# Optimization experiments

Measured on AMD Instinct MI355X. Metric: run time of the kernel, lower is better.

## Reference

```python
import jax, jax.numpy as jnp
import numpy as np

N = 100000
NEG_SLOPE = 0.2


def gat_conv(x, edge_index, W, att_src, att_dst, bias, heads, out_ch, concat):
    # x: [N, F_in]; W: [F_in, heads*out_ch]; att_*: [heads, out_ch]; bias per PyG
    h = (x @ W).reshape(N, heads, out_ch)  # [N, H, C]
    # add self loops (PyG default add_self_loops=True)
    loop = jnp.arange(N, dtype=edge_index.dtype)
    src = jnp.concatenate([edge_index[0], loop])  # [E+N]
    dst = jnp.concatenate([edge_index[1], loop])
    a_src = jnp.einsum('nhc,hc->nh', h, att_src)  # [N, H]
    a_dst = jnp.einsum('nhc,hc->nh', h, att_dst)
    e = jax.nn.leaky_relu(a_src[src] + a_dst[dst], NEG_SLOPE)  # [E+N, H]
    # segment softmax over destination nodes (numerically stable)
    m = jax.ops.segment_max(e, dst, num_segments=N)
    e = jnp.exp(e - m[dst])
    denom = jax.ops.segment_sum(e, dst, num_segments=N)
    alpha = e / (denom[dst] + 1e-16)  # [E+N, H]
    # weighted scatter-add aggregation
    out = jax.ops.segment_sum(h[src] * alpha[:, :, None], dst, num_segments=N)  # [N,H,C]
    if concat:
        out = out.reshape(N, heads * out_ch)
    else:
        out = out.mean(axis=1)
    return out + bias


def setup_inputs() -> dict:
    key = jax.random.key(0)
    ks = jax.random.split(key, 10)
    F_in, H1, C1, NCLS = 512, 8, 8, 40
    E = 1600000
    x = jax.random.normal(ks[0], (N, F_in), dtype=jnp.float32)
    edge_index = jax.random.randint(ks[1], (2, E), 0, N, dtype=jnp.int64)
    s1 = 1.0 / np.sqrt(F_in)
    s2 = 1.0 / np.sqrt(H1 * C1)
    return {
        'x': x,
        'edge_index': edge_index,
        'W1': jax.random.normal(ks[2], (F_in, H1 * C1), dtype=jnp.float32) * s1,
        'att_src1': jax.random.normal(ks[3], (H1, C1), dtype=jnp.float32) * 0.1,
        'att_dst1': jax.random.normal(ks[4], (H1, C1), dtype=jnp.float32) * 0.1,
        'b1': jnp.zeros((H1 * C1,), dtype=jnp.float32),
        'W2': jax.random.normal(ks[5], (H1 * C1, NCLS), dtype=jnp.float32) * s2,
        'att_src2': jax.random.normal(ks[6], (1, NCLS), dtype=jnp.float32) * 0.1,
        'att_dst2': jax.random.normal(ks[7], (1, NCLS), dtype=jnp.float32) * 0.1,
        'b2': jnp.zeros((NCLS,), dtype=jnp.float32),
    }


def reference(x, edge_index, W1, att_src1, att_dst1, b1, W2, att_src2, att_dst2, b2):
    # dropout in eval mode -> identity
    h = gat_conv(x, edge_index, W1, att_src1, att_dst1, b1, heads=8, out_ch=8, concat=True)
    h = jax.nn.elu(h)
    NCLS = W2.shape[1]
    out = gat_conv(h, edge_index, W2, att_src2, att_dst2, b2, heads=1, out_ch=NCLS, concat=False)
    return jax.nn.softmax(out, axis=1)
```

## Files before the change

### kernel.cpp

```cpp
#include <hip/hip_runtime.h>
#include <math.h>

#define N_NODES 100000
#define FIN     512
#define H1H     8
#define C1C     8
#define HC1     64
#define NCLS    40
#define NEG_SLOPE 0.2f

#define NPB   256
#define NBUK  391
#define EPB   4096

#define TM 64
#define BK 16
#define XPAD 68

__global__ __launch_bounds__(256) void k_gemm1(const float* __restrict__ x,
                                               const float* __restrict__ W1,
                                               const float* __restrict__ att_src,
                                               const float* __restrict__ att_dst,
                                               float* __restrict__ h1,
                                               float* __restrict__ a_src,
                                               float* __restrict__ a_dst) {
    __shared__ float xs[2][BK][XPAD];
    const int tx   = threadIdx.x;
    const int lane = tx & 63;
    const int wid  = __builtin_amdgcn_readfirstlane(tx >> 6);
    const int c0   = wid << 4;
    const int row_base = blockIdx.x * TM;
    const int gr   = row_base + lane;
    const bool valid = gr < N_NODES;

    const int sr  = tx >> 2;
    const int sk  = (tx & 3) << 2;
    const int sgr = row_base + sr;
    const bool svalid = sgr < N_NODES;

    float4 xr4;
    auto load_regs = [&](int k0) {
        xr4 = svalid ? *(const float4*)(x + (size_t)sgr * FIN + k0 + sk)
                     : make_float4(0.f, 0.f, 0.f, 0.f);
    };
    auto store_lds = [&](int buf) {
        xs[buf][sk + 0][sr] = xr4.x;
        xs[buf][sk + 1][sr] = xr4.y;
        xs[buf][sk + 2][sr] = xr4.z;
        xs[buf][sk + 3][sr] = xr4.w;
    };

    float acc[16];
#pragma unroll
    for (int j = 0; j < 16; j++) acc[j] = 0.f;

    load_regs(0);
    store_lds(0);
    __syncthreads();

    int buf = 0;
    for (int k0 = 0; k0 < FIN; k0 += BK, buf ^= 1) {
        const bool more = (k0 + BK < FIN);
        if (more) load_regs(k0 + BK);
#pragma unroll
        for (int k = 0; k < BK; k++) {
            const float xv = xs[buf][k][lane];
            const float* wr = W1 + (size_t)(k0 + k) * HC1 + c0;
#pragma unroll
            for (int j = 0; j < 16; j++)
                acc[j] = fmaf(xv, wr[j], acc[j]);
        }
        if (more) {
            store_lds(buf ^ 1);
            __syncthreads();
        }
    }

    float s0 = 0.f, s1 = 0.f, d0 = 0.f, d1 = 0.f;
#pragma unroll
    for (int j = 0; j < 8; j++) {
        s0 = fmaf(acc[j],     att_src[c0 + j],     s0);
        d0 = fmaf(acc[j],     att_dst[c0 + j],     d0);
        s1 = fmaf(acc[8 + j], att_src[c0 + 8 + j], s1);
        d1 = fmaf(acc[8 + j], att_dst[c0 + 8 + j], d1);
    }
    if (valid) {
#pragma unroll
        for (int t = 0; t < 4; t++)
            *(float4*)(h1 + (size_t)gr * HC1 + c0 + 4 * t) =
                make_float4(acc[4 * t], acc[4 * t + 1], acc[4 * t + 2], acc[4 * t + 3]);
        const int h0 = wid * 2;
        a_src[gr * H1H + h0]     = s0;
        a_src[gr * H1H + h0 + 1] = s1;
        a_dst[gr * H1H + h0]     = d0;
        a_dst[gr * H1H + h0 + 1] = d1;
    }
}

__global__ __launch_bounds__(256) void k_bcnt(const int* __restrict__ dst, int E,
                                              int* __restrict__ gcnt) {
    __shared__ int lcnt[NBUK];
    for (int i = threadIdx.x; i < NBUK; i += 256) lcnt[i] = 0;
    __syncthreads();
    const int e0 = blockIdx.x * EPB;
#pragma unroll
    for (int i = 0; i < EPB / 256; i++) {
        const int e = e0 + i * 256 + threadIdx.x;
        if (e < E) atomicAdd(&lcnt[dst[e] >> 8], 1);
    }
    __syncthreads();
    for (int i = threadIdx.x; i < NBUK; i += 256)
        if (lcnt[i]) atomicAdd(&gcnt[i], lcnt[i]);
}

__global__ __launch_bounds__(512) void k_bscan(const int* __restrict__ gcnt,
                                               int* __restrict__ gbase,
                                               int* __restrict__ gcur, int E) {
    __shared__ int sm[512];
    const int t = threadIdx.x;
    const int v = (t < NBUK) ? gcnt[t] : 0;
    sm[t] = v;
    __syncthreads();
    for (int off = 1; off < 512; off <<= 1) {
        const int u = (t >= off) ? sm[t - off] : 0;
        __syncthreads();
        sm[t] += u;
        __syncthreads();
    }
    if (t < NBUK) {
        const int b = sm[t] - v;
        gbase[t] = b;
        gcur[t]  = b;
    }
    if (t == 0) gbase[NBUK] = E;
}

__global__ __launch_bounds__(256) void k_bfill(const int* __restrict__ src,
                                               const int* __restrict__ dst, int E,
                                               int* __restrict__ gcur,
                                               int2* __restrict__ pairs) {
    __shared__ int lcnt[NBUK];
    __shared__ int lbase[NBUK];
    for (int i = threadIdx.x; i < NBUK; i += 256) lcnt[i] = 0;
    __syncthreads();
    const int e0 = blockIdx.x * EPB;
#pragma unroll
    for (int i = 0; i < EPB / 256; i++) {
        const int e = e0 + i * 256 + threadIdx.x;
        if (e < E) atomicAdd(&lcnt[dst[e] >> 8], 1);
    }
    __syncthreads();
    for (int i = threadIdx.x; i < NBUK; i += 256)
        lbase[i] = lcnt[i] ? atomicAdd(&gcur[i], lcnt[i]) : 0;
    __syncthreads();
#pragma unroll
    for (int i = 0; i < EPB / 256; i++) {
        const int e = e0 + i * 256 + threadIdx.x;
        if (e < E) {
            const int d = dst[e];
            const int pos = atomicAdd(&lbase[d >> 8], 1);
            pairs[pos] = make_int2(src[e], d);
        }
    }
}

__global__ __launch_bounds__(256) void k_bscatter(const int2* __restrict__ pairs,
                                                  const int* __restrict__ gbase,
                                                  int* __restrict__ offs,
                                                  int* __restrict__ srcsort, int E) {
    __shared__ int ldeg[NPB];
    __shared__ int ltmp[NPB];
    __shared__ int lcur[NPB];
    const int b = blockIdx.x;
    const int tx = threadIdx.x;
    const int node0 = b << 8;
    const int pbeg = gbase[b];
    const int cnt  = gbase[b + 1] - pbeg;

    ldeg[tx] = 0;
    __syncthreads();
    for (int i = tx; i < cnt; i += 256)
        atomicAdd(&ldeg[pairs[pbeg + i].y - node0], 1);
    __syncthreads();
    const int v = ldeg[tx];
    ltmp[tx] = v;
    __syncthreads();
    for (int off = 1; off < 256; off <<= 1) {
        const int u = (tx >= off) ? ltmp[tx - off] : 0;
        __syncthreads();
        ltmp[tx] += u;
        __syncthreads();
    }
    const int mypos = pbeg + ltmp[tx] - v;
    if (node0 + tx < N_NODES) offs[node0 + tx] = mypos;
    lcur[tx] = mypos;
    if (b == NBUK - 1 && tx == 0) offs[N_NODES] = E;
    __syncthreads();
    for (int i = tx; i < cnt; i += 256) {
        const int2 p = pairs[pbeg + i];
        const int pos = atomicAdd(&lcur[p.y - node0], 1);
        srcsort[pos] = p.x;
    }
}

__global__ __launch_bounds__(256) void k_agg1(const float* __restrict__ h1,
                                              const float* __restrict__ a_src,
                                              const float* __restrict__ a_dst,
                                              const int* __restrict__ offs,
                                              const int* __restrict__ srcsort,
                                              const float* __restrict__ b1,
                                              float* __restrict__ h1e) {
    const int n = blockIdx.x * 4 + (threadIdx.x >> 6);
    if (n >= N_NODES) return;
    const int lane = threadIdx.x & 63;
    const int hh   = lane >> 3;
    const float adn = a_dst[n * H1H + hh];
    const int beg = offs[n], end = offs[n + 1];

    float e0 = a_src[n * H1H + hh] + adn;
    e0 = e0 > 0.f ? e0 : NEG_SLOPE * e0;
    float m = e0;
    float denom = 1.f;
    float acc = h1[(size_t)n * HC1 + lane];

    int j = beg;
    for (; j + 8 <= end; j += 8) {
        int s[8];
#pragma unroll
        for (int t = 0; t < 8; t++) s[t] = srcsort[j + t];
        float q[8], g[8];
#pragma unroll
        for (int t = 0; t < 8; t++) q[t] = a_src[s[t] * H1H + hh];
#pragma unroll
        for (int t = 0; t < 8; t++) g[t] = h1[(size_t)s[t] * HC1 + lane];
        float f[8];
#pragma unroll
        for (int t = 0; t < 8; t++) {
            const float e = q[t] + adn;
            f[t] = e > 0.f ? e : NEG_SLOPE * e;
        }
        const float cm = fmaxf(fmaxf(fmaxf(f[0], f[1]), fmaxf(f[2], f[3])),
                               fmaxf(fmaxf(f[4], f[5]), fmaxf(f[6], f[7])));
        const float nm = fmaxf(m, cm);
        const float sc = __expf(m - nm);
        float w[8];
#pragma unroll
        for (int t = 0; t < 8; t++) w[t] = __expf(f[t] - nm);
        const float wsum = ((w[0] + w[1]) + (w[2] + w[3])) + ((w[4] + w[5]) + (w[6] + w[7]));
        const float wg = fmaf(w[0], g[0], fmaf(w[1], g[1], fmaf(w[2], g[2], fmaf(w[3], g[3],
                         fmaf(w[4], g[4], fmaf(w[5], g[5], fmaf(w[6], g[6], w[7] * g[7])))))));
        denom = fmaf(denom, sc, wsum);
        acc = fmaf(acc, sc, wg);
        m = nm;
    }
    for (; j + 4 <= end; j += 4) {
        const int s0 = srcsort[j], s1 = srcsort[j + 1];
        const int s2 = srcsort[j + 2], s3 = srcsort[j + 3];
        const float q0 = a_src[s0 * H1H + hh], q1 = a_src[s1 * H1H + hh];
        const float q2 = a_src[s2 * H1H + hh], q3 = a_src[s3 * H1H + hh];
        const float g0 = h1[(size_t)s0 * HC1 + lane];
        const float g1 = h1[(size_t)s1 * HC1 + lane];
        const float g2 = h1[(size_t)s2 * HC1 + lane];
        const float g3 = h1[(size_t)s3 * HC1 + lane];
        float f0 = q0 + adn; f0 = f0 > 0.f ? f0 : NEG_SLOPE * f0;
        float f1 = q1 + adn; f1 = f1 > 0.f ? f1 : NEG_SLOPE * f1;
        float f2 = q2 + adn; f2 = f2 > 0.f ? f2 : NEG_SLOPE * f2;
        float f3 = q3 + adn; f3 = f3 > 0.f ? f3 : NEG_SLOPE * f3;
        const float nm = fmaxf(m, fmaxf(fmaxf(f0, f1), fmaxf(f2, f3)));
        const float sc = __expf(m - nm);
        const float w0 = __expf(f0 - nm), w1 = __expf(f1 - nm);
        const float w2 = __expf(f2 - nm), w3 = __expf(f3 - nm);
        denom = fmaf(denom, sc, (w0 + w1) + (w2 + w3));
        acc = fmaf(acc, sc, fmaf(w0, g0, fmaf(w1, g1, fmaf(w2, g2, w3 * g3))));
        m = nm;
    }
    for (; j < end; j++) {
        const int s = srcsort[j];
        float e = a_src[s * H1H + hh] + adn;
        e = e > 0.f ? e : NEG_SLOPE * e;
        const float g = h1[(size_t)s * HC1 + lane];
        const float nm = fmaxf(m, e);
        const float sc = __expf(m - nm);
        const float w = __expf(e - nm);
        denom = fmaf(denom, sc, w);
        acc = fmaf(acc, sc, w * g);
        m = nm;
    }
    float v = acc / denom + b1[lane];
    h1e[(size_t)n * HC1 + lane] = v > 0.f ? v : (__expf(v) - 1.f);
}

#define TM2 128
__global__ __launch_bounds__(256) void k_gemm2(const float* __restrict__ h1e,
                                               const float* __restrict__ W2,
                                               const float* __restrict__ att_src2,
                                               const float* __restrict__ att_dst2,
                                               float* __restrict__ h2,
                                               float* __restrict__ a_src2,
                                               float* __restrict__ a_dst2) {
    __shared__ float hs[32][65][4];
    __shared__ float w2t[NCLS][68];
    __shared__ float asv[NCLS], adv[NCLS];
    const int tx = threadIdx.x;
    const int node0 = blockIdx.x * TM2;

    for (int f = tx; f < HC1 * NCLS; f += 256) {
        const int k = f / NCLS, c = f - k * NCLS;
        w2t[c][k] = W2[f];
    }
    if (tx < NCLS) {
        asv[tx] = att_src2[tx];
        adv[tx] = att_dst2[tx];
    }
#pragma unroll
    for (int i = 0; i < 8; i++) {
        const int f  = tx + 256 * i;
        const int n  = f >> 4;
        const int k4 = (f & 15) << 2;
        const int gn = node0 + n;
        const float4 v = (gn < N_NODES) ? *(const float4*)(h1e + (size_t)gn * HC1 + k4)
                                        : make_float4(0.f, 0.f, 0.f, 0.f);
        const int ng = n >> 2, ni = n & 3;
        hs[ng][k4 + 0][ni] = v.x;
        hs[ng][k4 + 1][ni] = v.y;
        hs[ng][k4 + 2][ni] = v.z;
        hs[ng][k4 + 3][ni] = v.w;
    }
    __syncthreads();

    const int ng = tx >> 3;
    const int cg = tx & 7;
    const int c0 = cg * 5;

    float acc[4][5];
#pragma unroll
    for (int i = 0; i < 4; i++)
#pragma unroll
        for (int j = 0; j < 5; j++) acc[i][j] = 0.f;

    for (int k = 0; k < HC1; k += 4) {
        float4 hv[4];
#pragma unroll
        for (int t = 0; t < 4; t++) hv[t] = *(const float4*)&hs[ng][k + t][0];
#pragma unroll
        for (int j = 0; j < 5; j++) {
            const float4 wv = *(const float4*)&w2t[c0 + j][k];
            acc[0][j] = fmaf(hv[0].x, wv.x, fmaf(hv[1].x, wv.y, fmaf(hv[2].x, wv.z, fmaf(hv[3].x, wv.w, acc[0][j]))));
            acc[1][j] = fmaf(hv[0].y, wv.x, fmaf(hv[1].y, wv.y, fmaf(hv[2].y, wv.z, fmaf(hv[3].y, wv.w, acc[1][j]))));
            acc[2][j] = fmaf(hv[0].z, wv.x, fmaf(hv[1].z, wv.y, fmaf(hv[2].z, wv.z, fmaf(hv[3].z, wv.w, acc[2][j]))));
            acc[3][j] = fmaf(hv[0].w, wv.x, fmaf(hv[1].w, wv.y, fmaf(hv[2].w, wv.z, fmaf(hv[3].w, wv.w, acc[3][j]))));
        }
    }

    float ps[4], pd[4];
#pragma unroll
    for (int i = 0; i < 4; i++) {
        const int gn = node0 + ng * 4 + i;
        float s = 0.f, d = 0.f;
#pragma unroll
        for (int j = 0; j < 5; j++) {
            s = fmaf(acc[i][j], asv[c0 + j], s);
            d = fmaf(acc[i][j], adv[c0 + j], d);
        }
        ps[i] = s;
        pd[i] = d;
        if (gn < N_NODES) {
#pragma unroll
            for (int j = 0; j < 5; j++)
                h2[(size_t)gn * NCLS + c0 + j] = acc[i][j];
        }
    }
#pragma unroll
    for (int off = 1; off < 8; off <<= 1) {
#pragma unroll
        for (int i = 0; i < 4; i++) {
            ps[i] += __shfl_xor(ps[i], off, 64);
            pd[i] += __shfl_xor(pd[i], off, 64);
        }
    }
    if (cg == 0) {
#pragma unroll
        for (int i = 0; i < 4; i++) {
            const int gn = node0 + ng * 4 + i;
            if (gn < N_NODES) {
                a_src2[gn] = ps[i];
                a_dst2[gn] = pd[i];
            }
        }
    }
}

__global__ __launch_bounds__(256) void k_agg2(const float* __restrict__ h2,
                                              const float* __restrict__ a_src,
                                              const float* __restrict__ a_dst,
                                              const int* __restrict__ offs,
                                              const int* __restrict__ srcsort,
                                              const float* __restrict__ b2,
                                              float* __restrict__ out) {
    const int n = blockIdx.x * 4 + (threadIdx.x >> 6);
    if (n >= N_NODES) return;
    const int lane = threadIdx.x & 63;
    const float adn = a_dst[n];
    const int beg = offs[n], end = offs[n + 1];

    float e0 = a_src[n] + adn;
    e0 = e0 > 0.f ? e0 : NEG_SLOPE * e0;
    float m = e0;
    float denom = 1.f;
    float acc = (lane < NCLS) ? h2[(size_t)n * NCLS + lane] : 0.f;

    int j = beg;
    for (; j + 8 <= end; j += 8) {
        int s[8];
#pragma unroll
        for (int t = 0; t < 8; t++) s[t] = srcsort[j + t];
        float q[8], g[8];
#pragma unroll
        for (int t = 0; t < 8; t++) q[t] = a_src[s[t]];
#pragma unroll
        for (int t = 0; t < 8; t++)
            g[t] = (lane < NCLS) ? h2[(size_t)s[t] * NCLS + lane] : 0.f;
        float f[8];
#pragma unroll
        for (int t = 0; t < 8; t++) {
            const float e = q[t] + adn;
            f[t] = e > 0.f ? e : NEG_SLOPE * e;
        }
        const float cm = fmaxf(fmaxf(fmaxf(f[0], f[1]), fmaxf(f[2], f[3])),
                               fmaxf(fmaxf(f[4], f[5]), fmaxf(f[6], f[7])));
        const float nm = fmaxf(m, cm);
        const float sc = __expf(m - nm);
        float w[8];
#pragma unroll
        for (int t = 0; t < 8; t++) w[t] = __expf(f[t] - nm);
        const float wsum = ((w[0] + w[1]) + (w[2] + w[3])) + ((w[4] + w[5]) + (w[6] + w[7]));
        const float wg = fmaf(w[0], g[0], fmaf(w[1], g[1], fmaf(w[2], g[2], fmaf(w[3], g[3],
                         fmaf(w[4], g[4], fmaf(w[5], g[5], fmaf(w[6], g[6], w[7] * g[7])))))));
        denom = fmaf(denom, sc, wsum);
        acc = fmaf(acc, sc, wg);
        m = nm;
    }
    for (; j + 4 <= end; j += 4) {
        const int s0 = srcsort[j], s1 = srcsort[j + 1];
        const int s2 = srcsort[j + 2], s3 = srcsort[j + 3];
        const float q0 = a_src[s0], q1 = a_src[s1];
        const float q2 = a_src[s2], q3 = a_src[s3];
        float g0 = 0.f, g1 = 0.f, g2 = 0.f, g3 = 0.f;
        if (lane < NCLS) {
            g0 = h2[(size_t)s0 * NCLS + lane];
            g1 = h2[(size_t)s1 * NCLS + lane];
            g2 = h2[(size_t)s2 * NCLS + lane];
            g3 = h2[(size_t)s3 * NCLS + lane];
        }
        float f0 = q0 + adn; f0 = f0 > 0.f ? f0 : NEG_SLOPE * f0;
        float f1 = q1 + adn; f1 = f1 > 0.f ? f1 : NEG_SLOPE * f1;
        float f2 = q2 + adn; f2 = f2 > 0.f ? f2 : NEG_SLOPE * f2;
        float f3 = q3 + adn; f3 = f3 > 0.f ? f3 : NEG_SLOPE * f3;
        const float nm = fmaxf(m, fmaxf(fmaxf(f0, f1), fmaxf(f2, f3)));
        const float sc = __expf(m - nm);
        const float w0 = __expf(f0 - nm), w1 = __expf(f1 - nm);
        const float w2 = __expf(f2 - nm), w3 = __expf(f3 - nm);
        denom = fmaf(denom, sc, (w0 + w1) + (w2 + w3));
        acc = fmaf(acc, sc, fmaf(w0, g0, fmaf(w1, g1, fmaf(w2, g2, w3 * g3))));
        m = nm;
    }
    for (; j < end; j++) {
        const int s = srcsort[j];
        float e = a_src[s] + adn;
        e = e > 0.f ? e : NEG_SLOPE * e;
        const float g = (lane < NCLS) ? h2[(size_t)s * NCLS + lane] : 0.f;
        const float nm = fmaxf(m, e);
        const float sc = __expf(m - nm);
        const float w = __expf(e - nm);
        denom = fmaf(denom, sc, w);
        acc = fmaf(acc, sc, w * g);
        m = nm;
    }
    float o = (lane < NCLS) ? (acc / denom + b2[lane]) : -INFINITY;
    float mx = o;
#pragma unroll
    for (int off = 32; off; off >>= 1) mx = fmaxf(mx, __shfl_xor(mx, off, 64));
    const float ex = (lane < NCLS) ? __expf(o - mx) : 0.f;
    float sm = ex;
#pragma unroll
    for (int off = 32; off; off >>= 1) sm += __shfl_xor(sm, off, 64);
    if (lane < NCLS) out[(size_t)n * NCLS + lane] = ex / sm;
}

extern "C" void kernel_launch(void* const* d_in, const int* in_sizes, int n_in,
                              void* d_out, int out_size, void* d_ws, size_t ws_size,
                              hipStream_t stream) {
    const float* x   = (const float*)d_in[0];
    const int*   ei  = (const int*)d_in[1];
    const float* W1v = (const float*)d_in[2];
    const float* as1 = (const float*)d_in[3];
    const float* ad1 = (const float*)d_in[4];
    const float* b1  = (const float*)d_in[5];
    const float* W2v = (const float*)d_in[6];
    const float* as2 = (const float*)d_in[7];
    const float* ad2 = (const float*)d_in[8];
    const float* b2  = (const float*)d_in[9];
    const int E = in_sizes[1] / 2;
    const int* esrc = ei;
    const int* edst = ei + E;

    char* wp = (char*)d_ws;
    auto alloc = [&](size_t bytes) {
        char* p = wp;
        wp += (bytes + 255) & ~(size_t)255;
        return p;
    };
    float* h1     = (float*)alloc((size_t)N_NODES * HC1 * 4);
    float* h1e    = (float*)alloc((size_t)N_NODES * HC1 * 4);
    float* a_src1 = (float*)alloc((size_t)N_NODES * H1H * 4);
    float* a_dst1 = (float*)alloc((size_t)N_NODES * H1H * 4);
    float* a_src2 = (float*)alloc((size_t)N_NODES * 4);
    float* a_dst2 = (float*)alloc((size_t)N_NODES * 4);
    int*   offs   = (int*)alloc((size_t)(N_NODES + 1) * 4);
    int*   gcnt   = (int*)alloc((size_t)NBUK * 4);
    int*   gbase  = (int*)alloc((size_t)(NBUK + 1) * 4);
    int*   gcur   = (int*)alloc((size_t)NBUK * 4);
    int*   srcsort= (int*)alloc((size_t)E * 4);
    int2*  pairs  = (int2*)alloc((size_t)E * 8);
    float* h2     = h1;

    hipMemsetAsync(gcnt, 0, (size_t)NBUK * 4, stream);

    const int NEB = (E + EPB - 1) / EPB;
    k_gemm1<<<(N_NODES + TM - 1) / TM, 256, 0, stream>>>(x, W1v, as1, ad1, h1, a_src1, a_dst1);
    k_bcnt<<<NEB, 256, 0, stream>>>(edst, E, gcnt);
    k_bscan<<<1, 512, 0, stream>>>(gcnt, gbase, gcur, E);
    k_bfill<<<NEB, 256, 0, stream>>>(esrc, edst, E, gcur, pairs);
    k_bscatter<<<NBUK, 256, 0, stream>>>(pairs, gbase, offs, srcsort, E);
    k_agg1<<<(N_NODES + 3) / 4, 256, 0, stream>>>(h1, a_src1, a_dst1, offs, srcsort, b1, h1e);
    k_gemm2<<<(N_NODES + TM2 - 1) / TM2, 256, 0, stream>>>(h1e, W2v, as2, ad2, h2, a_src2, a_dst2);
    k_agg2<<<(N_NODES + 3) / 4, 256, 0, stream>>>(h2, a_src2, a_dst2, offs, srcsort, b2, (float*)d_out);
}
```

Baseline: 661.2 us.

## Register-tile first-layer GEMM with 16x8 outputs per thread and LDS-staged weights

Rewrites the first projection GEMM so each thread computes a 16-row by 8-column register tile. The block tile grows to 256 rows with 128 threads, and both x and W1 are staged in double-buffered LDS with padded, swizzled rows. Before, every thread read 16 W1 values from global memory per k step and did only 16 FMAs per LDS load; the new tiling raises FMA-to-load intensity. The cost is heavy register pressure (128 accumulators), fewer blocks (391) and lower occupancy.

Measured after the change: 654.9 us. Within noise of the previous version (-0.9%).

```diff
diff --git a/kernel.cpp b/kernel.cpp
--- a/kernel.cpp
+++ b/kernel.cpp
@@ -13,46 +13,63 @@
 #define NBUK  391
 #define EPB   4096
 
-#define TM 64
-#define BK 16
-#define XPAD 68
-
-__global__ __launch_bounds__(256) void k_gemm1(const float* __restrict__ x,
+#define TM 256
+#define BK 8
+#define XSW 320
+
+__global__ __launch_bounds__(128) void k_gemm1(const float* __restrict__ x,
                                                const float* __restrict__ W1,
                                                const float* __restrict__ att_src,
                                                const float* __restrict__ att_dst,
                                                float* __restrict__ h1,
                                                float* __restrict__ a_src,
                                                float* __restrict__ a_dst) {
-    __shared__ float xs[2][BK][XPAD];
-    const int tx   = threadIdx.x;
-    const int lane = tx & 63;
-    const int wid  = __builtin_amdgcn_readfirstlane(tx >> 6);
-    const int c0   = wid << 4;
+    __shared__ float xs[2][BK][XSW];
+    __shared__ float ws[2][BK][68];
+    const int t = threadIdx.x;
     const int row_base = blockIdx.x * TM;
-    const int gr   = row_base + lane;
-    const bool valid = gr < N_NODES;
-
-    const int sr  = tx >> 2;
-    const int sk  = (tx & 3) << 2;
-    const int sgr = row_base + sr;
-    const bool svalid = sgr < N_NODES;
-
-    float4 xr4;
+    const int rg = t >> 3;
+    const int cg = t & 7;
+    const int xbase = rg * 20;
+
+    int srow[4], skq[4];
+#pragma unroll
+    for (int i = 0; i < 4; i++) {
+        const int f = t + 128 * i;
+        srow[i] = f >> 1;
+        skq[i]  = (f & 1) << 2;
+    }
+    const int wkk = t >> 4;
+    const int wc4 = (t & 15) << 2;
+
+    float4 xr4[4];
+    float4 wr4;
     auto load_regs = [&](int k0) {
-        xr4 = svalid ? *(const float4*)(x + (size_t)sgr * FIN + k0 + sk)
-                     : make_float4(0.f, 0.f, 0.f, 0.f);
+#pragma unroll
+        for (int i = 0; i < 4; i++) {
+            const int gr = row_base + srow[i];
+            xr4[i] = (gr < N_NODES) ? *(const float4*)(x + (size_t)gr * FIN + k0 + skq[i])
+                                    : make_float4(0.f, 0.f, 0.f, 0.f);
+        }
+        wr4 = *(const float4*)(W1 + (size_t)(k0 + wkk) * HC1 + wc4);
     };
     auto store_lds = [&](int buf) {
-        xs[buf][sk + 0][sr] = xr4.x;
-        xs[buf][sk + 1][sr] = xr4.y;
-        xs[buf][sk + 2][sr] = xr4.z;
-        xs[buf][sk + 3][sr] = xr4.w;
+#pragma unroll
+        for (int i = 0; i < 4; i++) {
+            const int rp = srow[i] + ((srow[i] >> 4) << 2);
+            xs[buf][skq[i] + 0][rp] = xr4[i].x;
+            xs[buf][skq[i] + 1][rp] = xr4[i].y;
+            xs[buf][skq[i] + 2][rp] = xr4[i].z;
+            xs[buf][skq[i] + 3][rp] = xr4[i].w;
+        }
+        *(float4*)&ws[buf][wkk][wc4] = wr4;
     };
 
-    float acc[16];
-#pragma unroll
-    for (int j = 0; j < 16; j++) acc[j] = 0.f;
+    float acc[16][8];
+#pragma unroll
+    for (int i = 0; i < 16; i++)
+#pragma unroll
+        for (int j = 0; j < 8; j++) acc[i][j] = 0.f;
 
     load_regs(0);
     store_lds(0);
@@ -64,11 +81,23 @@
         if (more) load_regs(k0 + BK);
 #pragma unroll
         for (int k = 0; k < BK; k++) {
-            const float xv = xs[buf][k][lane];
-            const float* wr = W1 + (size_t)(k0 + k) * HC1 + c0;
-#pragma unroll
-            for (int j = 0; j < 16; j++)
-                acc[j] = fmaf(xv, wr[j], acc[j]);
+            const float4 xa0 = *(const float4*)&xs[buf][k][xbase];
+            const float4 xa1 = *(const float4*)&xs[buf][k][xbase + 4];
+            const float4 xa2 = *(const float4*)&xs[buf][k][xbase + 8];
+            const float4 xa3 = *(const float4*)&xs[buf][k][xbase + 12];
+            const float4 wv0 = *(const float4*)&ws[buf][k][cg * 8];
+            const float4 wv1 = *(const float4*)&ws[buf][k][cg * 8 + 4];
+            const float xr[16] = {xa0.x, xa0.y, xa0.z, xa0.w,
+                                  xa1.x, xa1.y, xa1.z, xa1.w,
+                                  xa2.x, xa2.y, xa2.z, xa2.w,
+                                  xa3.x, xa3.y, xa3.z, xa3.w};
+            const float wr[8] = {wv0.x, wv0.y, wv0.z, wv0.w,
+                                 wv1.x, wv1.y, wv1.z, wv1.w};
+#pragma unroll
+            for (int i = 0; i < 16; i++)
+#pragma unroll
+                for (int j = 0; j < 8; j++)
+                    acc[i][j] = fmaf(xr[i], wr[j], acc[i][j]);
         }
         if (more) {
             store_lds(buf ^ 1);
@@ -76,24 +105,29 @@
         }
     }
 
-    float s0 = 0.f, s1 = 0.f, d0 = 0.f, d1 = 0.f;
+    float asv[8], adv[8];
 #pragma unroll
     for (int j = 0; j < 8; j++) {
-        s0 = fmaf(acc[j],     att_src[c0 + j],     s0);
-        d0 = fmaf(acc[j],     att_dst[c0 + j],     d0);
-        s1 = fmaf(acc[8 + j], att_src[c0 + 8 + j], s1);
-        d1 = fmaf(acc[8 + j], att_dst[c0 + 8 + j], d1);
-    }
-    if (valid) {
-#pragma unroll
-        for (int t = 0; t < 4; t++)
-            *(float4*)(h1 + (size_t)gr * HC1 + c0 + 4 * t) =
-                make_float4(acc[4 * t], acc[4 * t + 1], acc[4 * t + 2], acc[4 * t + 3]);
-        const int h0 = wid * 2;
-        a_src[gr * H1H + h0]     = s0;
-        a_src[gr * H1H + h0 + 1] = s1;
-        a_dst[gr * H1H + h0]     = d0;
-        a_dst[gr * H1H + h0 + 1] = d1;
+        asv[j] = att_src[cg * 8 + j];
+        adv[j] = att_dst[cg * 8 + j];
+    }
+#pragma unroll
+    for (int i = 0; i < 16; i++) {
+        const int gr = row_base + rg * 16 + i;
+        if (gr < N_NODES) {
+            *(float4*)(h1 + (size_t)gr * HC1 + cg * 8) =
+                make_float4(acc[i][0], acc[i][1], acc[i][2], acc[i][3]);
+            *(float4*)(h1 + (size_t)gr * HC1 + cg * 8 + 4) =
+                make_float4(acc[i][4], acc[i][5], acc[i][6], acc[i][7]);
+            float s = 0.f, d = 0.f;
+#pragma unroll
+            for (int j = 0; j < 8; j++) {
+                s = fmaf(acc[i][j], asv[j], s);
+                d = fmaf(acc[i][j], adv[j], d);
+            }
+            a_src[gr * H1H + cg] = s;
+            a_dst[gr * H1H + cg] = d;
+        }
     }
 }
 
@@ -527,7 +561,7 @@
     hipMemsetAsync(gcnt, 0, (size_t)NBUK * 4, stream);
 
     const int NEB = (E + EPB - 1) / EPB;
-    k_gemm1<<<(N_NODES + TM - 1) / TM, 256, 0, stream>>>(x, W1v, as1, ad1, h1, a_src1, a_dst1);
+    k_gemm1<<<(N_NODES + TM - 1) / TM, 128, 0, stream>>>(x, W1v, as1, ad1, h1, a_src1, a_dst1);
     k_bcnt<<<NEB, 256, 0, stream>>>(edst, E, gcnt);
     k_bscan<<<1, 512, 0, stream>>>(gcnt, gbase, gcur, E);
     k_bfill<<<NEB, 256, 0, stream>>>(esrc, edst, E, gcur, pairs);
```
